# Optimization experiments

Hardware: AMD Instinct MI355X
Metric: run time of the kernel (lower is better)

The kernel has to match this reference:

```python
import jax, jax.numpy as jnp
import numpy as np

N = 12500      # nodes
E = 200000     # edges (avg degree 16)
IN = 32        # inp_dim
OUT = 32       # out_dim
ATTN = 32      # attn_rel_emb_dim
R = 200        # num_rels
NB = 50        # num_bases


def setup_inputs() -> dict:
    key = jax.random.key(0)
    ks = jax.random.split(key, 10)
    node_feat = jax.random.normal(ks[0], (N, IN), jnp.float32)
    total_edge = jax.random.randint(ks[1], (2, E), 0, N)
    total_target_relation = jax.random.normal(ks[2], (E, ATTN), jnp.float32)
    total_relation_embed = jax.random.normal(ks[3], (E, ATTN), jnp.float32)
    total_relation = jax.random.randint(ks[4], (E,), 0, R)
    # learned parameters (xavier-ish scale)
    weight = jax.random.normal(ks[5], (NB, IN, OUT), jnp.float32) * 0.1
    w_comp = jax.random.normal(ks[6], (R, NB), jnp.float32) * 0.1
    self_loop_weight = jax.random.normal(ks[7], (IN, OUT), jnp.float32) * 0.1
    A_w = jax.random.normal(ks[8], (IN, 2 * IN + 2 * ATTN), jnp.float32) * 0.1
    A_b = jnp.zeros((IN,), jnp.float32)
    B_w = jax.random.normal(ks[9], (1, IN), jnp.float32) * 0.1
    B_b = jnp.zeros((1,), jnp.float32)
    return {
        'node_feat': node_feat,
        'total_target_relation': total_target_relation,
        'total_relation_embed': total_relation_embed,
        'weight': weight,
        'w_comp': w_comp,
        'self_loop_weight': self_loop_weight,
        'A_w': A_w,
        'A_b': A_b,
        'B_w': B_w,
        'B_b': B_b,
        'total_edge': total_edge,
        'total_relation': total_relation,
    }


def reference(node_feat, total_target_relation, total_relation_embed,
              weight, w_comp, self_loop_weight, A_w, A_b, B_w, B_b,
              total_edge, total_relation):
    # basis decomposition: per-relation weight [R, IN, OUT]
    rel_w = jnp.einsum('rb,bio->rio', w_comp, weight)
    src = node_feat[total_edge[0]]            # [E, IN]
    tgt = node_feat[total_edge[1]]            # [E, IN]
    # per-edge relation-specific transform (bmm in torch)
    msg = jnp.einsum('ei,eio->eo', src, rel_w[total_relation])  # [E, OUT]
    curr = tgt @ self_loop_weight             # [E, OUT]
    # attention MLP: sigmoid(B(relu(A(concat))))
    e = jnp.concatenate([src, tgt, total_relation_embed, total_target_relation], axis=1)
    h = jax.nn.relu(e @ A_w.T + A_b)
    a = jax.nn.sigmoid(h @ B_w.T + B_b)       # [E, 1]
    curr = curr + msg * a
    # gnn_spmm(e2n_sp, curr): scatter-add edge messages to target nodes
    out = jax.ops.segment_sum(curr, total_edge[1], num_segments=node_feat.shape[0])
    return out  # [N, OUT]
```

## Files before the change

### kernel.cpp

```cpp
#include <hip/hip_runtime.h>

#define N_NODES 12500
#define N_EDGES 200000
#define DIM 32
#define N_REL 200
#define N_BASES 50

#define OUT_ELEMS   (N_NODES * DIM)
#define ZERO_BLOCKS ((OUT_ELEMS + 1023) / 1024)

#define EDGES_PER_HBLOCK 1024
#define HIST_BLOCKS ((N_EDGES + EDGES_PER_HBLOCK - 1) / EDGES_PER_HBLOCK)

#define AWBF_OFF  409600
#define SLWT_OFF  417792
#define BINS_OFF  419840
#define GCUR_OFF  420640
#define PERM_OFF  421440
#define WS_A (PERM_OFF + N_EDGES * 16)
#define WS_B (PERM_OFF + N_EDGES * 4)

typedef __attribute__((ext_vector_type(8))) short short8;
typedef __attribute__((ext_vector_type(4))) float f32x4;
typedef __attribute__((ext_vector_type(4))) unsigned short us4;

__device__ __forceinline__ unsigned short f2bf(float x) {
    union { float f; unsigned u; } v; v.f = x;
    unsigned r = (v.u + 0x7FFFu + ((v.u >> 16) & 1u)) >> 16;
    return (unsigned short)r;
}
__device__ __forceinline__ float bf2f(unsigned short u) {
    return __uint_as_float(((unsigned)u) << 16);
}

__device__ __forceinline__ short8 cvt8(float4 a, float4 b) {
    short8 r;
    r[0] = (short)f2bf(a.x); r[1] = (short)f2bf(a.y);
    r[2] = (short)f2bf(a.z); r[3] = (short)f2bf(a.w);
    r[4] = (short)f2bf(b.x); r[5] = (short)f2bf(b.y);
    r[6] = (short)f2bf(b.z); r[7] = (short)f2bf(b.w);
    return r;
}

__device__ __forceinline__ int clampi(int x, int hi) {
    return x < 0 ? 0 : (x >= hi ? hi - 1 : x);
}

#define MFMA(A, B, C) __builtin_amdgcn_mfma_f32_16x16x32_bf16(A, B, C, 0, 0, 0)

__global__ __launch_bounds__(256) void prep_kernel(
    const float* __restrict__ weight,
    const float* __restrict__ w_comp,
    const float* __restrict__ Aw,
    const float* __restrict__ slw,
    const int*  __restrict__ rel,
    unsigned short* __restrict__ relw_bf,
    unsigned short* __restrict__ aw_bf,
    unsigned short* __restrict__ slwT_bf,
    int* __restrict__ bins,
    float* __restrict__ out,
    int sorted)
{
    int b = blockIdx.x, tid = threadIdx.x;
    if (b < N_REL) {
        __shared__ float wc[N_BASES];
        if (tid < N_BASES) wc[tid] = w_comp[b * N_BASES + tid];
        __syncthreads();
        const float* wp = weight + tid * 4;
        float4 acc = make_float4(0.f, 0.f, 0.f, 0.f);
        #pragma unroll 10
        for (int bb = 0; bb < N_BASES; bb++) {
            float4 w = *(const float4*)(wp + bb * 1024);
            float c = wc[bb];
            acc.x = fmaf(c, w.x, acc.x); acc.y = fmaf(c, w.y, acc.y);
            acc.z = fmaf(c, w.z, acc.z); acc.w = fmaf(c, w.w, acc.w);
        }
        int i = (tid * 4) >> 5, o = (tid * 4) & 31;
        if (sorted) {
            relw_bf[b * 1024 + (o + 0) * 32 + i] = f2bf(acc.x);
            relw_bf[b * 1024 + (o + 1) * 32 + i] = f2bf(acc.y);
            relw_bf[b * 1024 + (o + 2) * 32 + i] = f2bf(acc.z);
            relw_bf[b * 1024 + (o + 3) * 32 + i] = f2bf(acc.w);
        } else {
            us4 ov;
            ov[0] = f2bf(acc.x); ov[1] = f2bf(acc.y);
            ov[2] = f2bf(acc.z); ov[3] = f2bf(acc.w);
            *(us4*)(relw_bf + b * 1024 + tid * 4) = ov;
        }
    } else if (b < N_REL + ZERO_BLOCKS) {
        int base = (b - N_REL) * 1024 + tid * 4;
        if (base + 3 < OUT_ELEMS)
            *(float4*)(out + base) = make_float4(0.f, 0.f, 0.f, 0.f);
        else
            for (int k = 0; k < 4; k++)
                if (base + k < OUT_ELEMS) out[base + k] = 0.f;
    } else if (b == N_REL + ZERO_BLOCKS) {
        for (int x = tid; x < 32 * 128; x += 256) aw_bf[x] = f2bf(Aw[x]);
        for (int x = tid; x < 32 * 32; x += 256) {
            int i = x >> 5, j = x & 31;
            slwT_bf[j * 32 + i] = f2bf(slw[x]);
        }
    } else {
        __shared__ int lb[N_REL];
        if (tid < N_REL) lb[tid] = 0;
        __syncthreads();
        int base = (b - (N_REL + ZERO_BLOCKS + 1)) * EDGES_PER_HBLOCK + tid;
        #pragma unroll
        for (int k = 0; k < 4; k++) {
            int e = base + k * 256;
            if (e < N_EDGES) atomicAdd(&lb[clampi(rel[e], N_REL)], 1);
        }
        __syncthreads();
        if (tid < N_REL && lb[tid] > 0) atomicAdd(&bins[tid], lb[tid]);
    }
}

__global__ __launch_bounds__(256) void scatter_kernel(
    const int* __restrict__ rel,
    const int* __restrict__ edge0,
    const int* __restrict__ edge1,
    const int* __restrict__ bins,
    int* __restrict__ gcur,
    int4* __restrict__ perm4,
    int* __restrict__ permi)
{
    __shared__ int sb[N_REL];
    __shared__ int pref[N_REL];
    __shared__ int lb[N_REL];
    int tid = threadIdx.x;
    if (tid < N_REL) { sb[tid] = bins[tid]; lb[tid] = 0; }
    __syncthreads();
    if (tid == 0) {
        int run = 0;
        for (int r = 0; r < N_REL; r++) { pref[r] = run; run += sb[r]; }
    }
    __syncthreads();
    int base = blockIdx.x * EDGES_PER_HBLOCK + tid;
    int myr[4], myrank[4];
    #pragma unroll
    for (int k = 0; k < 4; k++) {
        int e = base + k * 256;
        myr[k] = -1;
        if (e < N_EDGES) {
            myr[k] = clampi(rel[e], N_REL);
            myrank[k] = atomicAdd(&lb[myr[k]], 1);
        }
    }
    __syncthreads();
    if (tid < N_REL) {
        int c = lb[tid];
        lb[tid] = c > 0 ? (pref[tid] + atomicAdd(&gcur[tid], c)) : 0;
    }
    __syncthreads();
    #pragma unroll
    for (int k = 0; k < 4; k++) {
        if (myr[k] >= 0) {
            int e = base + k * 256;
            int pos = lb[myr[k]] + myrank[k];
            if (perm4) {
                int s = clampi(edge0[e], N_NODES);
                int t = clampi(edge1[e], N_NODES);
                perm4[pos] = make_int4(s, t, myr[k], e);
            } else {
                permi[pos] = e;
            }
        }
    }
}

__global__ __launch_bounds__(256) void edge_kernel(
    const float* __restrict__ node_feat,
    const float* __restrict__ ttr,
    const float* __restrict__ tre,
    const float* __restrict__ Ab,
    const float* __restrict__ Bw,
    const float* __restrict__ Bb,
    const int*  __restrict__ edge0,
    const int*  __restrict__ edge1,
    const int*  __restrict__ rel,
    const int4* __restrict__ perm4,
    const int*  __restrict__ permi,
    const unsigned short* __restrict__ relw_bf,
    const unsigned short* __restrict__ aw_bf,
    const unsigned short* __restrict__ slwT_bf,
    float* __restrict__ out)
{
    __shared__ float msgL[4 * 16 * 36];

    int tid  = threadIdx.x;
    int wave = tid >> 6;
    int lane = tid & 63;
    int m = lane & 15;
    int q = lane >> 4;
    int base = blockIdx.x * 256 + wave * 64;
    if (base >= N_EDGES) return;

    bool sorted = (perm4 != nullptr) || (permi != nullptr);

    int s_l, t_l, r_l, e_l;
    if (perm4) {
        int4 pv = perm4[base + lane];
        s_l = pv.x; t_l = pv.y; r_l = pv.z; e_l = pv.w;
    } else {
        int eid = permi ? clampi(permi[base + lane], N_EDGES) : (base + lane);
        e_l = eid;
        s_l = clampi(edge0[eid], N_NODES);
        t_l = clampi(edge1[eid], N_NODES);
        r_l = clampi(rel[eid],   N_REL);
    }

    short8 bA[4][2], bS[2];
    #pragma unroll
    for (int hh = 0; hh < 2; hh++) {
        #pragma unroll
        for (int c = 0; c < 4; c++)
            bA[c][hh] = *(const short8*)(aw_bf + (16 * hh + m) * 128 + 32 * c + 8 * q);
        bS[hh] = *(const short8*)(slwT_bf + (16 * hh + m) * 32 + 8 * q);
    }
    float ab0 = Ab[m], ab1 = Ab[16 + m];
    float bw0 = Bw[m], bw1 = Bw[16 + m], Bb0 = Bb[0];

    int r0 = __shfl(r_l, 0, 64);
    bool uniWave = sorted && __all(r_l == r0);
    short8 bM0w = {}, bM1w = {};
    if (uniWave) {
        const unsigned short* rwt = relw_bf + r0 * 1024;
        bM0w = *(const short8*)(rwt + m * 32 + 8 * q);
        bM1w = *(const short8*)(rwt + (16 + m) * 32 + 8 * q);
    }

    #pragma unroll
    for (int sb = 0; sb < 4; sb++) {
        int lb = sb * 16;
        int s_m   = __shfl(s_l, lb + m, 64);
        int t_m   = __shfl(t_l, lb + m, 64);
        int eid_m = __shfl(e_l, lb + m, 64);

        const float* sp = node_feat + s_m * DIM + q * 8;
        float4 sv0 = *(const float4*)sp, sv1 = *(const float4*)(sp + 4);
        const float* tp = node_feat + t_m * DIM + q * 8;
        float4 tv0 = *(const float4*)tp, tv1 = *(const float4*)(tp + 4);
        const float* rp = tre + eid_m * DIM + q * 8;
        float4 rv0 = *(const float4*)rp, rv1 = *(const float4*)(rp + 4);
        const float* qp = ttr + eid_m * DIM + q * 8;
        float4 qv0 = *(const float4*)qp, qv1 = *(const float4*)(qp + 4);

        short8 fsrc = cvt8(sv0, sv1);
        short8 ftgt = cvt8(tv0, tv1);
        short8 fre  = cvt8(rv0, rv1);
        short8 ftr  = cvt8(qv0, qv1);

        f32x4 hacc0 = {ab0, ab0, ab0, ab0};
        f32x4 hacc1 = {ab1, ab1, ab1, ab1};
        f32x4 cacc0 = {0.f, 0.f, 0.f, 0.f};
        f32x4 cacc1 = {0.f, 0.f, 0.f, 0.f};

        hacc0 = MFMA(fsrc, bA[0][0], hacc0);  hacc1 = MFMA(fsrc, bA[0][1], hacc1);
        hacc0 = MFMA(ftgt, bA[1][0], hacc0);  hacc1 = MFMA(ftgt, bA[1][1], hacc1);
        hacc0 = MFMA(fre,  bA[2][0], hacc0);  hacc1 = MFMA(fre,  bA[2][1], hacc1);
        hacc0 = MFMA(ftr,  bA[3][0], hacc0);  hacc1 = MFMA(ftr,  bA[3][1], hacc1);
        cacc0 = MFMA(ftgt, bS[0], cacc0);     cacc1 = MFMA(ftgt, bS[1], cacc1);

        f32x4 macc0 = {0.f, 0.f, 0.f, 0.f};
        f32x4 macc1 = {0.f, 0.f, 0.f, 0.f};
        int r_sb = __shfl(r_l, lb + m, 64);
        int r00  = __shfl(r_l, lb, 64);
        bool uni = uniWave || (sorted && __all(r_sb == r00));
        if (uni) {
            short8 bM0 = bM0w, bM1 = bM1w;
            if (!uniWave) {
                const unsigned short* rwt = relw_bf + r00 * 1024;
                bM0 = *(const short8*)(rwt + m * 32 + 8 * q);
                bM1 = *(const short8*)(rwt + (16 + m) * 32 + 8 * q);
            }
            macc0 = MFMA(fsrc, bM0, macc0);
            macc1 = MFMA(fsrc, bM1, macc1);
        } else {
            int e_loc = lane >> 2;
            int cq    = lane & 3;
            int r_e = __shfl(r_l, lb + e_loc, 64);
            float sf[8] = {sv0.x, sv0.y, sv0.z, sv0.w, sv1.x, sv1.y, sv1.z, sv1.w};
            float msg[8] = {0.f, 0.f, 0.f, 0.f, 0.f, 0.f, 0.f, 0.f};
            const unsigned short* rw = relw_bf + r_e * 1024;
            #pragma unroll 4
            for (int k = 0; k < 32; k++) {
                float s_k = __shfl(sf[k & 7], e_loc + 16 * (k >> 3), 64);
                if (sorted) {
                    #pragma unroll
                    for (int p = 0; p < 8; p++)
                        msg[p] = fmaf(s_k, bf2f(rw[(cq * 8 + p) * 32 + k]), msg[p]);
                } else {
                    union { short8 s; unsigned u[4]; } W;
                    W.s = *(const short8*)(rw + k * 32 + cq * 8);
                    #pragma unroll
                    for (int p = 0; p < 4; p++) {
                        msg[2 * p]     = fmaf(s_k, __uint_as_float(W.u[p] << 16), msg[2 * p]);
                        msg[2 * p + 1] = fmaf(s_k, __uint_as_float(W.u[p] & 0xffff0000u), msg[2 * p + 1]);
                    }
                }
            }
            float* ml = msgL + wave * (16 * 36);
            *(float4*)(ml + e_loc * 36 + cq * 8)     = make_float4(msg[0], msg[1], msg[2], msg[3]);
            *(float4*)(ml + e_loc * 36 + cq * 8 + 4) = make_float4(msg[4], msg[5], msg[6], msg[7]);
            #pragma unroll
            for (int v = 0; v < 4; v++) {
                macc0[v] = ml[(4 * q + v) * 36 + m];
                macc1[v] = ml[(4 * q + v) * 36 + 16 + m];
            }
        }

        float av[4];
        #pragma unroll
        for (int v = 0; v < 4; v++) {
            float p = fmaxf(hacc0[v], 0.f) * bw0 + fmaxf(hacc1[v], 0.f) * bw1;
            p += __shfl_xor(p, 1, 16);
            p += __shfl_xor(p, 2, 16);
            p += __shfl_xor(p, 4, 16);
            p += __shfl_xor(p, 8, 16);
            av[v] = 1.f / (1.f + __expf(-(p + Bb0)));
        }
        #pragma unroll
        for (int v = 0; v < 4; v++) {
            int row = 4 * q + v;
            int tv = __shfl(t_l, lb + row, 64);
            atomicAdd(&out[tv * DIM + m],      cacc0[v] + macc0[v] * av[v]);
            atomicAdd(&out[tv * DIM + 16 + m], cacc1[v] + macc1[v] * av[v]);
        }
    }
}

extern "C" void kernel_launch(void* const* d_in, const int* in_sizes, int n_in,
                              void* d_out, int out_size, void* d_ws, size_t ws_size,
                              hipStream_t stream) {
    const float* node_feat = (const float*)d_in[0];
    const float* ttr       = (const float*)d_in[1];
    const float* tre       = (const float*)d_in[2];
    const float* weight    = (const float*)d_in[3];
    const float* w_comp    = (const float*)d_in[4];
    const float* slw       = (const float*)d_in[5];
    const float* Aw        = (const float*)d_in[6];
    const float* Ab        = (const float*)d_in[7];
    const float* Bw        = (const float*)d_in[8];
    const float* Bb        = (const float*)d_in[9];
    const int*  total_edge = (const int*)d_in[10];
    const int*  rel        = (const int*)d_in[11];
    const int*  edge0 = total_edge;
    const int*  edge1 = total_edge + N_EDGES;

    unsigned short* relw_bf = (unsigned short*)d_ws;
    unsigned short* aw_bf   = (unsigned short*)((char*)d_ws + AWBF_OFF);
    unsigned short* slwT_bf = (unsigned short*)((char*)d_ws + SLWT_OFF);
    int* bins = (int*)((char*)d_ws + BINS_OFF);
    int* gcur = (int*)((char*)d_ws + GCUR_OFF);
    float* out = (float*)d_out;

    int tierA = ws_size >= (size_t)WS_A;
    int tierB = !tierA && ws_size >= (size_t)WS_B;
    int sorted = tierA || tierB;
    int4* perm4 = tierA ? (int4*)((char*)d_ws + PERM_OFF) : nullptr;
    int*  permi = tierB ? (int*)((char*)d_ws + PERM_OFF) : nullptr;

    if (sorted) hipMemsetAsync(bins, 0, 1600, stream);

    int prep_blocks = N_REL + ZERO_BLOCKS + 1 + (sorted ? HIST_BLOCKS : 0);
    prep_kernel<<<prep_blocks, 256, 0, stream>>>(
        weight, w_comp, Aw, slw, rel, relw_bf, aw_bf, slwT_bf, bins, out, sorted);

    if (sorted)
        scatter_kernel<<<HIST_BLOCKS, 256, 0, stream>>>(
            rel, edge0, edge1, bins, gcur, perm4, permi);

    edge_kernel<<<(N_EDGES + 255) / 256, 256, 0, stream>>>(
        node_feat, ttr, tre, Ab, Bw, Bb,
        edge0, edge1, rel, perm4, permi,
        relw_bf, aw_bf, slwT_bf, out);
}
```

Measured before the change: 153.2 us.

## Accumulate scatter-add in packed bf16 atomics with a final fp32 conversion pass

```diff
diff --git a/kernel.cpp b/kernel.cpp
--- a/kernel.cpp
+++ b/kernel.cpp
@@ -7,7 +7,7 @@
 #define N_BASES 50
 
 #define OUT_ELEMS   (N_NODES * DIM)
-#define ZERO_BLOCKS ((OUT_ELEMS + 1023) / 1024)
+#define ACCZ_BLOCKS 196
 
 #define EDGES_PER_HBLOCK 1024
 #define HIST_BLOCKS ((N_EDGES + EDGES_PER_HBLOCK - 1) / EDGES_PER_HBLOCK)
@@ -16,13 +16,15 @@
 #define SLWT_OFF  417792
 #define BINS_OFF  419840
 #define GCUR_OFF  420640
-#define PERM_OFF  421440
+#define ACC_OFF   421440
+#define PERM_OFF  1221440
 #define WS_A (PERM_OFF + N_EDGES * 16)
 #define WS_B (PERM_OFF + N_EDGES * 4)
 
 typedef __attribute__((ext_vector_type(8))) short short8;
 typedef __attribute__((ext_vector_type(4))) float f32x4;
 typedef __attribute__((ext_vector_type(4))) unsigned short us4;
+typedef __attribute__((ext_vector_type(2))) short bf2v;
 
 __device__ __forceinline__ unsigned short f2bf(float x) {
     union { float f; unsigned u; } v; v.f = x;
@@ -31,6 +33,18 @@
 }
 __device__ __forceinline__ float bf2f(unsigned short u) {
     return __uint_as_float(((unsigned)u) << 16);
+}
+
+__device__ __forceinline__ void pk_atomic_bf16(unsigned short* p, float lo, float hi) {
+    bf2v v; v[0] = (short)f2bf(lo); v[1] = (short)f2bf(hi);
+#if __has_builtin(__builtin_amdgcn_global_atomic_fadd_v2bf16)
+    typedef __attribute__((address_space(1))) bf2v gbf2v;
+    __builtin_amdgcn_global_atomic_fadd_v2bf16((gbf2v*)(unsigned long long)p, v);
+#else
+    union { bf2v v2; unsigned u; } pk; pk.v2 = v;
+    asm volatile("global_atomic_pk_add_bf16 %0, %1, off"
+                 :: "v"(p), "v"(pk.u) : "memory");
+#endif
 }
 
 __device__ __forceinline__ short8 cvt8(float4 a, float4 b) {
@@ -58,7 +72,7 @@
     unsigned short* __restrict__ aw_bf,
     unsigned short* __restrict__ slwT_bf,
     int* __restrict__ bins,
-    float* __restrict__ out,
+    unsigned short* __restrict__ acc,
     int sorted)
 {
     int b = blockIdx.x, tid = threadIdx.x;
@@ -67,34 +81,31 @@
         if (tid < N_BASES) wc[tid] = w_comp[b * N_BASES + tid];
         __syncthreads();
         const float* wp = weight + tid * 4;
-        float4 acc = make_float4(0.f, 0.f, 0.f, 0.f);
+        float4 acc4 = make_float4(0.f, 0.f, 0.f, 0.f);
         #pragma unroll 10
         for (int bb = 0; bb < N_BASES; bb++) {
             float4 w = *(const float4*)(wp + bb * 1024);
             float c = wc[bb];
-            acc.x = fmaf(c, w.x, acc.x); acc.y = fmaf(c, w.y, acc.y);
-            acc.z = fmaf(c, w.z, acc.z); acc.w = fmaf(c, w.w, acc.w);
+            acc4.x = fmaf(c, w.x, acc4.x); acc4.y = fmaf(c, w.y, acc4.y);
+            acc4.z = fmaf(c, w.z, acc4.z); acc4.w = fmaf(c, w.w, acc4.w);
         }
         int i = (tid * 4) >> 5, o = (tid * 4) & 31;
         if (sorted) {
-            relw_bf[b * 1024 + (o + 0) * 32 + i] = f2bf(acc.x);
-            relw_bf[b * 1024 + (o + 1) * 32 + i] = f2bf(acc.y);
-            relw_bf[b * 1024 + (o + 2) * 32 + i] = f2bf(acc.z);
-            relw_bf[b * 1024 + (o + 3) * 32 + i] = f2bf(acc.w);
+            relw_bf[b * 1024 + (o + 0) * 32 + i] = f2bf(acc4.x);
+            relw_bf[b * 1024 + (o + 1) * 32 + i] = f2bf(acc4.y);
+            relw_bf[b * 1024 + (o + 2) * 32 + i] = f2bf(acc4.z);
+            relw_bf[b * 1024 + (o + 3) * 32 + i] = f2bf(acc4.w);
         } else {
             us4 ov;
-            ov[0] = f2bf(acc.x); ov[1] = f2bf(acc.y);
-            ov[2] = f2bf(acc.z); ov[3] = f2bf(acc.w);
+            ov[0] = f2bf(acc4.x); ov[1] = f2bf(acc4.y);
+            ov[2] = f2bf(acc4.z); ov[3] = f2bf(acc4.w);
             *(us4*)(relw_bf + b * 1024 + tid * 4) = ov;
         }
-    } else if (b < N_REL + ZERO_BLOCKS) {
-        int base = (b - N_REL) * 1024 + tid * 4;
-        if (base + 3 < OUT_ELEMS)
-            *(float4*)(out + base) = make_float4(0.f, 0.f, 0.f, 0.f);
-        else
-            for (int k = 0; k < 4; k++)
-                if (base + k < OUT_ELEMS) out[base + k] = 0.f;
-    } else if (b == N_REL + ZERO_BLOCKS) {
+    } else if (b < N_REL + ACCZ_BLOCKS) {
+        int idx = (b - N_REL) * 256 + tid;
+        if (idx < (OUT_ELEMS * 2 / 16))
+            ((uint4*)acc)[idx] = make_uint4(0u, 0u, 0u, 0u);
+    } else if (b == N_REL + ACCZ_BLOCKS) {
         for (int x = tid; x < 32 * 128; x += 256) aw_bf[x] = f2bf(Aw[x]);
         for (int x = tid; x < 32 * 32; x += 256) {
             int i = x >> 5, j = x & 31;
@@ -104,7 +115,7 @@
         __shared__ int lb[N_REL];
         if (tid < N_REL) lb[tid] = 0;
         __syncthreads();
-        int base = (b - (N_REL + ZERO_BLOCKS + 1)) * EDGES_PER_HBLOCK + tid;
+        int base = (b - (N_REL + ACCZ_BLOCKS + 1)) * EDGES_PER_HBLOCK + tid;
         #pragma unroll
         for (int k = 0; k < 4; k++) {
             int e = base + k * 256;
@@ -183,7 +194,7 @@
     const unsigned short* __restrict__ relw_bf,
     const unsigned short* __restrict__ aw_bf,
     const unsigned short* __restrict__ slwT_bf,
-    float* __restrict__ out)
+    unsigned short* __restrict__ acc)
 {
     __shared__ float msgL[4 * 16 * 36];
 
@@ -323,9 +334,27 @@
         for (int v = 0; v < 4; v++) {
             int row = 4 * q + v;
             int tv = __shfl(t_l, lb + row, 64);
-            atomicAdd(&out[tv * DIM + m],      cacc0[v] + macc0[v] * av[v]);
-            atomicAdd(&out[tv * DIM + 16 + m], cacc1[v] + macc1[v] * av[v]);
-        }
+            float val0 = cacc0[v] + macc0[v] * av[v];
+            float val1 = cacc1[v] + macc1[v] * av[v];
+            float o0 = __shfl_xor(val0, 1, 64);
+            float o1 = __shfl_xor(val1, 1, 64);
+            bool ev = (m & 1) == 0;
+            int col  = ev ? m : (m + 15);
+            float lo = ev ? val0 : o1;
+            float hi = ev ? o0 : val1;
+            pk_atomic_bf16(acc + tv * DIM + col, lo, hi);
+        }
+    }
+}
+
+__global__ __launch_bounds__(256) void cvt_kernel(
+    const unsigned short* __restrict__ acc, float* __restrict__ out)
+{
+    int i = (blockIdx.x * 256 + threadIdx.x) * 4;
+    if (i < OUT_ELEMS) {
+        us4 a = *(const us4*)(acc + i);
+        float4 o = make_float4(bf2f(a[0]), bf2f(a[1]), bf2f(a[2]), bf2f(a[3]));
+        *(float4*)(out + i) = o;
     }
 }
 
@@ -352,6 +381,7 @@
     unsigned short* slwT_bf = (unsigned short*)((char*)d_ws + SLWT_OFF);
     int* bins = (int*)((char*)d_ws + BINS_OFF);
     int* gcur = (int*)((char*)d_ws + GCUR_OFF);
+    unsigned short* acc = (unsigned short*)((char*)d_ws + ACC_OFF);
     float* out = (float*)d_out;
 
     int tierA = ws_size >= (size_t)WS_A;
@@ -362,9 +392,9 @@
 
     if (sorted) hipMemsetAsync(bins, 0, 1600, stream);
 
-    int prep_blocks = N_REL + ZERO_BLOCKS + 1 + (sorted ? HIST_BLOCKS : 0);
+    int prep_blocks = N_REL + ACCZ_BLOCKS + 1 + (sorted ? HIST_BLOCKS : 0);
     prep_kernel<<<prep_blocks, 256, 0, stream>>>(
-        weight, w_comp, Aw, slw, rel, relw_bf, aw_bf, slwT_bf, bins, out, sorted);
+        weight, w_comp, Aw, slw, rel, relw_bf, aw_bf, slwT_bf, bins, acc, sorted);
 
     if (sorted)
         scatter_kernel<<<HIST_BLOCKS, 256, 0, stream>>>(
@@ -373,5 +403,7 @@
     edge_kernel<<<(N_EDGES + 255) / 256, 256, 0, stream>>>(
         node_feat, ttr, tre, Ab, Bw, Bb,
         edge0, edge1, rel, perm4, permi,
-        relw_bf, aw_bf, slwT_bf, out);
-}
+        relw_bf, aw_bf, slwT_bf, acc);
+
+    cvt_kernel<<<(OUT_ELEMS / 4 + 255) / 256, 256, 0, stream>>>(acc, out);
+}
```

After: 156.3 us. Within noise of the previous version (+2.0%).
